# Performance work log

Measured on AMD Instinct MI355X. Metric: run time of the kernel, lower is better.

The kernel has to match this reference:

```python
import jax, jax.numpy as jnp
import numpy as np

N, E, D, H = 50000, 800000, 128, 8
C = D // H  # per-head out_channels = 16
NEG_SLOPE = 0.2
EPS = 1e-5


def _layer_norm(x, w):
    mu = x.mean(-1, keepdims=True)
    var = ((x - mu) ** 2).mean(-1, keepdims=True)
    return (x - mu) / jnp.sqrt(var + EPS) * w


def setup_inputs() -> dict:
    key = jax.random.key(0)
    ks = jax.random.split(key, 9)
    s = 0.05  # weight init scale
    return {
        "x": jax.random.normal(ks[0], (N, D), dtype=jnp.float32),
        "edge_index": jax.random.randint(ks[1], (2, E), 0, N, dtype=jnp.int32),
        "edge_attr": jax.random.normal(ks[2], (E, D), dtype=jnp.float32),
        "ln1_w": jnp.ones((D,), jnp.float32),
        "lin_l_w": jax.random.normal(ks[3], (D, D), dtype=jnp.float32) * s,
        "lin_l_b": jnp.zeros((D,), jnp.float32),
        "lin_r_w": jax.random.normal(ks[4], (D, D), dtype=jnp.float32) * s,
        "lin_r_b": jnp.zeros((D,), jnp.float32),
        "lin_edge_w": jax.random.normal(ks[5], (D, D), dtype=jnp.float32) * s,
        "att": jax.random.normal(ks[6], (H, C), dtype=jnp.float32) * s,
        "attn_bias": jnp.zeros((D,), jnp.float32),
        "ln2_w": jnp.ones((D,), jnp.float32),
        "fc_w": jax.random.normal(ks[7], (4 * D, D), dtype=jnp.float32) * s,
        "proj_w": jax.random.normal(ks[8], (D, 4 * D), dtype=jnp.float32) * s,
    }


def reference(x, edge_index, edge_attr, ln1_w, lin_l_w, lin_l_b, lin_r_w,
              lin_r_b, lin_edge_w, att, attn_bias, ln2_w, fc_w, proj_w):
    n, d = x.shape
    h_heads, c = att.shape
    # --- GATv2Conv on ln_1(x) ---
    h = _layer_norm(x, ln1_w)
    xl = (h @ lin_l_w.T + lin_l_b).reshape(n, h_heads, c)  # source transform
    xr = (h @ lin_r_w.T + lin_r_b).reshape(n, h_heads, c)  # target transform
    e = (edge_attr @ lin_edge_w.T).reshape(-1, h_heads, c)  # [E,H,C]
    src, dst = edge_index[0], edge_index[1]
    z = jax.nn.leaky_relu(xl[src] + xr[dst] + e, NEG_SLOPE)  # [E,H,C]
    logits = jnp.einsum('ehc,hc->eh', z, att)  # [E,H]
    # segment softmax over destination nodes
    m = jax.lax.stop_gradient(jax.ops.segment_max(logits, dst, num_segments=n))
    num = jnp.exp(logits - m[dst])
    den = jax.ops.segment_sum(num, dst, num_segments=n)
    alpha = num / den[dst]  # [E,H]
    msg = xl[src] * alpha[..., None]  # [E,H,C]
    attn_out = jax.ops.segment_sum(msg, dst, num_segments=n).reshape(n, d) + attn_bias
    x = x + attn_out
    # --- MLP on ln_2(x) ---
    h2 = _layer_norm(x, ln2_w)
    x = x + jax.nn.relu(h2 @ fc_w.T) @ proj_w.T
    return x
```

## Files before the change

### kernel.cpp

```cpp
#include <hip/hip_runtime.h>

#define D 128
#define HEADS 8
#define CH 16
#define NEG 0.2f
#define LNEPS 1e-5f

typedef __attribute__((ext_vector_type(8))) short bf16x8;
typedef __attribute__((ext_vector_type(4))) float f32x4;

#define MFMA(a, b, c) __builtin_amdgcn_mfma_f32_16x16x32_bf16(a, b, c, 0, 0, 0)

__device__ __forceinline__ short f2bf(float f) {
    unsigned u = __builtin_bit_cast(unsigned, f);
    unsigned r = (u + 0x7fffu + ((u >> 16) & 1u)) >> 16;
    return (short)r;
}
__device__ __forceinline__ float bflo(unsigned u) {
    return __builtin_bit_cast(float, u << 16);
}
__device__ __forceinline__ float bfhi(unsigned u) {
    return __builtin_bit_cast(float, u & 0xffff0000u);
}
__device__ __forceinline__ bf16x8 pack8(f32x4 lo, f32x4 hi) {
    bf16x8 r;
    r[0] = f2bf(lo[0]); r[1] = f2bf(lo[1]); r[2] = f2bf(lo[2]); r[3] = f2bf(lo[3]);
    r[4] = f2bf(hi[0]); r[5] = f2bf(hi[1]); r[6] = f2bf(hi[2]); r[7] = f2bf(hi[3]);
    return r;
}

__global__ void convert_weights(const float* __restrict__ wl, const float* __restrict__ wr,
                                const float* __restrict__ we, const float* __restrict__ fc,
                                const float* __restrict__ pj, short* __restrict__ out) {
    int idx = blockIdx.x * 256 + threadIdx.x;
    float v;
    if (idx < 16384) v = wl[idx];
    else if (idx < 32768) v = wr[idx - 16384];
    else if (idx < 49152) v = we[idx - 32768];
    else if (idx < 114688) v = fc[idx - 49152];
    else if (idx < 180224) v = pj[idx - 114688];
    else return;
    out[idx] = f2bf(v);
}

__global__ void ln_kernel(const float* __restrict__ x, const float* __restrict__ w,
                          short* __restrict__ h, int n) {
    int row = blockIdx.x * 4 + (threadIdx.x >> 6);
    if (row >= n) return;
    int l = threadIdx.x & 63;
    long base = (long)row * D;
    float a = x[base + l], b = x[base + l + 64];
    float s = a + b, ss = a * a + b * b;
    #pragma unroll
    for (int m = 1; m < 64; m <<= 1) { s += __shfl_xor(s, m); ss += __shfl_xor(ss, m); }
    float mu = s * (1.0f / 128.0f);
    float var = ss * (1.0f / 128.0f) - mu * mu;
    float rstd = rsqrtf(var + LNEPS);
    h[base + l]      = f2bf((a - mu) * rstd * w[l]);
    h[base + l + 64] = f2bf((b - mu) * rstd * w[l + 64]);
}

__global__ __launch_bounds__(256) void node_lin_kernel(
        const short* __restrict__ h, const short* __restrict__ wl, const short* __restrict__ wr,
        const float* __restrict__ bl, const float* __restrict__ br,
        short* __restrict__ xl, short* __restrict__ xr, int n) {
    int wave = threadIdx.x >> 6, l = threadIdx.x & 63;
    int rbase = blockIdx.x * 64 + wave * 16;
    int g = l >> 4, c = l & 15;
    f32x4 acc[16];
    #pragma unroll
    for (int t = 0; t < 16; t++) acc[t] = (f32x4){0.f, 0.f, 0.f, 0.f};
    int arow = rbase + c;
    #pragma unroll
    for (int kk = 0; kk < 4; kk++) {
        int k0 = kk * 32 + g * 8;
        bf16x8 af = {};
        if (arow < n) af = *(const bf16x8*)(h + (long)arow * D + k0);
        #pragma unroll
        for (int t = 0; t < 16; t++) {
            const short* w = (t < 8) ? wl : wr;
            int col = (t & 7) * 16 + c;
            bf16x8 bf = *(const bf16x8*)(w + col * D + k0);
            acc[t] = MFMA(af, bf, acc[t]);
        }
    }
    #pragma unroll
    for (int t = 0; t < 16; t++) {
        int col = (t & 7) * 16 + c;
        short* out = (t < 8) ? xl : xr;
        float bias = (t < 8) ? bl[col] : br[col];
        #pragma unroll
        for (int r = 0; r < 4; r++) {
            int row = rbase + g * 4 + r;
            if (row < n) out[(long)row * D + col] = f2bf(acc[t][r] + bias);
        }
    }
}

__global__ void hist_kernel(const int* __restrict__ dst, int* __restrict__ counts, int nE) {
    int e = blockIdx.x * 256 + threadIdx.x;
    if (e < nE) atomicAdd(&counts[dst[e]], 1);
}

__global__ void scan1_kernel(const int* __restrict__ counts, int* __restrict__ offsets,
                             int* __restrict__ blocksum, int n) {
    __shared__ int sd[1024];
    int tid = threadIdx.x;
    int gid = blockIdx.x * 1024 + tid;
    int v = (gid < n) ? counts[gid] : 0;
    sd[tid] = v;
    __syncthreads();
    int acc = v;
    #pragma unroll
    for (int off = 1; off < 1024; off <<= 1) {
        int t = (tid >= off) ? sd[tid - off] : 0;
        __syncthreads();
        acc += t;
        sd[tid] = acc;
        __syncthreads();
    }
    if (gid < n) offsets[gid] = acc - v;
    if (tid == 1023) blocksum[blockIdx.x] = acc;
}

__global__ void scan2_kernel(int* __restrict__ blocksum, int nb) {
    __shared__ int sd[256];
    int tid = threadIdx.x;
    int v = (tid < nb) ? blocksum[tid] : 0;
    sd[tid] = v;
    __syncthreads();
    int acc = v;
    #pragma unroll
    for (int off = 1; off < 256; off <<= 1) {
        int t = (tid >= off) ? sd[tid - off] : 0;
        __syncthreads();
        acc += t;
        sd[tid] = acc;
        __syncthreads();
    }
    if (tid < nb) blocksum[tid] = acc - v;
}

__global__ void scan3_kernel(int* __restrict__ offsets, const int* __restrict__ blocksum,
                             int* __restrict__ cursor, int n) {
    int gid = blockIdx.x * 256 + threadIdx.x;
    if (gid < n) {
        int o = offsets[gid] + blocksum[gid >> 10];
        offsets[gid] = o;
        cursor[gid] = o;
    }
}

__global__ void place_kernel(const int* __restrict__ src, const int* __restrict__ dst,
                             int* __restrict__ cursor, int* __restrict__ posOf,
                             int* __restrict__ src_perm, int nE) {
    int e = blockIdx.x * 256 + threadIdx.x;
    if (e < nE) {
        int pos = atomicAdd(&cursor[dst[e]], 1);
        posOf[e] = pos;
        src_perm[pos] = src[e];
    }
}

__global__ __launch_bounds__(256) void edge_kernel(
        const float* __restrict__ ea, const short* __restrict__ we,
        const int* __restrict__ src, const int* __restrict__ dst,
        const int* __restrict__ posOf,
        const short* __restrict__ xl, const short* __restrict__ xr,
        const float* __restrict__ att, float* __restrict__ num_perm,
        int nE, int ntiles, int nwaves) {
    __shared__ short wlds[16384];
    int tid = threadIdx.x;

    {
        int row = tid >> 1, half = tid & 1;
        const short* srow = we + row * D + half * 64;
        #pragma unroll
        for (int j = 0; j < 8; j++) {
            bf16x8 v = *(const bf16x8*)(srow + j * 8);
            int off = (half * 128 + j * 16) ^ ((row & 15) << 4);
            *(bf16x8*)((char*)wlds + row * 256 + off) = v;
        }
    }
    __syncthreads();

    int wave = tid >> 6, l = tid & 63;
    int el = l & 15, g = l >> 4;
    long ti = (long)blockIdx.x * 4 + wave;
    if (ti >= ntiles) return;

    int s, d, pos;
    f32x4 ear[8];
    {
        long e0 = ti * 16 + el;
        long ec = (e0 < nE) ? e0 : (nE - 1);
        s = src[ec]; d = dst[ec]; pos = posOf[ec];
        const float* p = ea + ec * D + g * 8;
        ear[0] = *(const f32x4*)(p);       ear[1] = *(const f32x4*)(p + 4);
        ear[2] = *(const f32x4*)(p + 32);  ear[3] = *(const f32x4*)(p + 36);
        ear[4] = *(const f32x4*)(p + 64);  ear[5] = *(const f32x4*)(p + 68);
        ear[6] = *(const f32x4*)(p + 96);  ear[7] = *(const f32x4*)(p + 100);
    }

    for (; ti < ntiles; ti += nwaves) {
        bool valid = (ti * 16 + el) < nE;
        int sc = s, dc = d, pc = pos;

        uint2 gl[8], gr[8];
        #pragma unroll
        for (int t = 0; t < 8; t++) {
            gl[t] = *(const uint2*)(xl + (long)sc * D + t * CH + g * 4);
            gr[t] = *(const uint2*)(xr + (long)dc * D + t * CH + g * 4);
        }

        long tin = ti + nwaves;
        long tcl = (tin < ntiles) ? tin : ti;
        long ecn;
        {
            long en = tcl * 16 + el;
            ecn = (en < nE) ? en : (nE - 1);
            s = src[ecn]; d = dst[ecn]; pos = posOf[ecn];
        }

        bf16x8 b0 = pack8(ear[0], ear[1]);
        bf16x8 b1 = pack8(ear[2], ear[3]);
        bf16x8 b2 = pack8(ear[4], ear[5]);
        bf16x8 b3 = pack8(ear[6], ear[7]);

        {
            const float* p = ea + ecn * D + g * 8;
            ear[0] = *(const f32x4*)(p);       ear[1] = *(const f32x4*)(p + 4);
            ear[2] = *(const f32x4*)(p + 32);  ear[3] = *(const f32x4*)(p + 36);
            ear[4] = *(const f32x4*)(p + 64);  ear[5] = *(const f32x4*)(p + 68);
            ear[6] = *(const f32x4*)(p + 96);  ear[7] = *(const f32x4*)(p + 100);
        }

        f32x4 acc[8];
        #pragma unroll
        for (int t = 0; t < 8; t++) acc[t] = (f32x4){0.f, 0.f, 0.f, 0.f};
        #pragma unroll
        for (int kk = 0; kk < 4; kk++) {
            bf16x8 bb = (kk == 0) ? b0 : (kk == 1) ? b1 : (kk == 2) ? b2 : b3;
            #pragma unroll
            for (int t = 0; t < 8; t++) {
                int row = t * CH + el;
                int off = row * 256 + ((kk * 64 + g * 16) ^ ((row & 15) << 4));
                bf16x8 af = *(const bf16x8*)((char*)wlds + off);
                acc[t] = MFMA(af, bb, acc[t]);
            }
        }

        float logit[8];
        #pragma unroll
        for (int t = 0; t < 8; t++) {
            f32x4 av = *(const f32x4*)(att + t * CH + g * 4);
            float v0 = acc[t][0] + bflo(gl[t].x) + bflo(gr[t].x);
            float v1 = acc[t][1] + bfhi(gl[t].x) + bfhi(gr[t].x);
            float v2 = acc[t][2] + bflo(gl[t].y) + bflo(gr[t].y);
            float v3 = acc[t][3] + bfhi(gl[t].y) + bfhi(gr[t].y);
            v0 = v0 > 0.f ? v0 : NEG * v0;
            v1 = v1 > 0.f ? v1 : NEG * v1;
            v2 = v2 > 0.f ? v2 : NEG * v2;
            v3 = v3 > 0.f ? v3 : NEG * v3;
            float lg = v0 * av[0];
            lg = fmaf(v1, av[1], lg);
            lg = fmaf(v2, av[2], lg);
            lg = fmaf(v3, av[3], lg);
            lg += __shfl_xor(lg, 16);
            lg += __shfl_xor(lg, 32);
            logit[t] = lg;
        }
        if (g == 0 && valid) {
            float4 o0 = make_float4(__expf(logit[0]), __expf(logit[1]),
                                    __expf(logit[2]), __expf(logit[3]));
            float4 o1 = make_float4(__expf(logit[4]), __expf(logit[5]),
                                    __expf(logit[6]), __expf(logit[7]));
            *(float4*)(num_perm + (long)pc * HEADS) = o0;
            *(float4*)(num_perm + (long)pc * HEADS + 4) = o1;
        }
    }
}

__global__ __launch_bounds__(256) void aggregate_kernel(
        const int* __restrict__ src_perm, const int* __restrict__ offsets,
        const int* __restrict__ counts, const float* __restrict__ num_perm,
        const short* __restrict__ xl, const float* __restrict__ x,
        const float* __restrict__ ab, const float* __restrict__ w2,
        float* __restrict__ x_mid, short* __restrict__ h2, int n) {
    int node = blockIdx.x * 4 + (threadIdx.x >> 6);
    if (node >= n) return;
    int l = threadIdx.x & 63;
    int h = l >> 3;
    int start = offsets[node], cnt = counts[node];
    float a0 = 0.f, a1 = 0.f, den = 0.f;
    int i = 0;
    for (; i + 4 <= cnt; i += 4) {
        int s0 = src_perm[start + i],     s1 = src_perm[start + i + 1];
        int s2 = src_perm[start + i + 2], s3 = src_perm[start + i + 3];
        float n0 = num_perm[(long)(start + i) * HEADS + h];
        float n1 = num_perm[(long)(start + i + 1) * HEADS + h];
        float n2 = num_perm[(long)(start + i + 2) * HEADS + h];
        float n3 = num_perm[(long)(start + i + 3) * HEADS + h];
        unsigned u0 = *(const unsigned*)(xl + (long)s0 * D + 2 * l);
        unsigned u1 = *(const unsigned*)(xl + (long)s1 * D + 2 * l);
        unsigned u2 = *(const unsigned*)(xl + (long)s2 * D + 2 * l);
        unsigned u3 = *(const unsigned*)(xl + (long)s3 * D + 2 * l);
        a0 = fmaf(bflo(u0), n0, a0); a1 = fmaf(bfhi(u0), n0, a1);
        a0 = fmaf(bflo(u1), n1, a0); a1 = fmaf(bfhi(u1), n1, a1);
        a0 = fmaf(bflo(u2), n2, a0); a1 = fmaf(bfhi(u2), n2, a1);
        a0 = fmaf(bflo(u3), n3, a0); a1 = fmaf(bfhi(u3), n3, a1);
        den += n0 + n1 + n2 + n3;
    }
    for (; i < cnt; i++) {
        float nm = num_perm[(long)(start + i) * HEADS + h];
        int s = src_perm[start + i];
        unsigned u = *(const unsigned*)(xl + (long)s * D + 2 * l);
        a0 = fmaf(bflo(u), nm, a0);
        a1 = fmaf(bfhi(u), nm, a1);
        den += nm;
    }
    float rden = cnt > 0 ? 1.f / den : 0.f;
    a0 *= rden; a1 *= rden;
    long base = (long)node * D;
    float2 xv = *(const float2*)(x + base + 2 * l);
    float2 abv = *(const float2*)(ab + 2 * l);
    float xm0 = xv.x + a0 + abv.x;
    float xm1 = xv.y + a1 + abv.y;
    *(float2*)(x_mid + base + 2 * l) = make_float2(xm0, xm1);
    float s_ = xm0 + xm1, ss = xm0 * xm0 + xm1 * xm1;
    #pragma unroll
    for (int m = 1; m < 64; m <<= 1) { s_ += __shfl_xor(s_, m); ss += __shfl_xor(ss, m); }
    float mu = s_ * (1.0f / 128.0f);
    float var = ss * (1.0f / 128.0f) - mu * mu;
    float rstd = rsqrtf(var + LNEPS);
    float2 wv = *(const float2*)(w2 + 2 * l);
    h2[base + 2 * l]     = f2bf((xm0 - mu) * rstd * wv.x);
    h2[base + 2 * l + 1] = f2bf((xm1 - mu) * rstd * wv.y);
}

__global__ __launch_bounds__(256) void fc_kernel(const short* __restrict__ h2,
                                                 const short* __restrict__ wfc,
                                                 short* __restrict__ t512, int n) {
    int wave = threadIdx.x >> 6, l = threadIdx.x & 63;
    int rbase = blockIdx.x * 64 + wave * 16;
    int cbase = blockIdx.y * 256;
    int g = l >> 4, c = l & 15;
    f32x4 acc[16];
    #pragma unroll
    for (int t = 0; t < 16; t++) acc[t] = (f32x4){0.f, 0.f, 0.f, 0.f};
    int arow = rbase + c;
    #pragma unroll
    for (int kk = 0; kk < 4; kk++) {
        int k0 = kk * 32 + g * 8;
        bf16x8 af = {};
        if (arow < n) af = *(const bf16x8*)(h2 + (long)arow * D + k0);
        #pragma unroll
        for (int t = 0; t < 16; t++) {
            int col = cbase + t * 16 + c;
            bf16x8 bf = *(const bf16x8*)(wfc + (long)col * D + k0);
            acc[t] = MFMA(af, bf, acc[t]);
        }
    }
    #pragma unroll
    for (int t = 0; t < 16; t++) {
        int col = cbase + t * 16 + c;
        #pragma unroll
        for (int r = 0; r < 4; r++) {
            int row = rbase + g * 4 + r;
            if (row < n) {
                float v = acc[t][r];
                t512[(long)row * 512 + col] = f2bf(v > 0.f ? v : 0.f);
            }
        }
    }
}

__global__ __launch_bounds__(256) void proj_kernel(const short* __restrict__ t512,
                                                   const short* __restrict__ wpj,
                                                   const float* __restrict__ x_mid,
                                                   float* __restrict__ out, int n) {
    int wave = threadIdx.x >> 6, l = threadIdx.x & 63;
    int rbase = blockIdx.x * 64 + wave * 16;
    int g = l >> 4, c = l & 15;
    f32x4 acc[8];
    #pragma unroll
    for (int t = 0; t < 8; t++) acc[t] = (f32x4){0.f, 0.f, 0.f, 0.f};
    int arow = rbase + c;
    #pragma unroll
    for (int kk = 0; kk < 16; kk++) {
        int k0 = kk * 32 + g * 8;
        bf16x8 af = {};
        if (arow < n) af = *(const bf16x8*)(t512 + (long)arow * 512 + k0);
        #pragma unroll
        for (int t = 0; t < 8; t++) {
            bf16x8 bf = *(const bf16x8*)(wpj + (long)(t * 16 + c) * 512 + k0);
            acc[t] = MFMA(af, bf, acc[t]);
        }
    }
    #pragma unroll
    for (int t = 0; t < 8; t++) {
        int col = t * 16 + c;
        #pragma unroll
        for (int r = 0; r < 4; r++) {
            int row = rbase + g * 4 + r;
            if (row < n) out[(long)row * D + col] = x_mid[(long)row * D + col] + acc[t][r];
        }
    }
}

extern "C" void kernel_launch(void* const* d_in, const int* in_sizes, int n_in,
                              void* d_out, int out_size, void* d_ws, size_t ws_size,
                              hipStream_t stream) {
    const float* x    = (const float*)d_in[0];
    const int*   eidx = (const int*)d_in[1];
    const float* ea   = (const float*)d_in[2];
    const float* ln1w = (const float*)d_in[3];
    const float* wl   = (const float*)d_in[4];
    const float* bl   = (const float*)d_in[5];
    const float* wr   = (const float*)d_in[6];
    const float* br   = (const float*)d_in[7];
    const float* we   = (const float*)d_in[8];
    const float* att  = (const float*)d_in[9];
    const float* ab   = (const float*)d_in[10];
    const float* ln2w = (const float*)d_in[11];
    const float* wfc  = (const float*)d_in[12];
    const float* wpj  = (const float*)d_in[13];
    int N = in_sizes[0] / D;
    int E = in_sizes[1] / 2;
    const int* srcp = eidx;
    const int* dstp = eidx + E;

    char* ws = (char*)d_ws;
    size_t NB2 = (size_t)N * D * 2;
    size_t NB4 = (size_t)N * D * 4;
    size_t E84 = (size_t)E * HEADS * 4;
    size_t o = 0;
    short* xl_bf   = (short*)(ws + o); o += NB2;
    short* xr_bf   = (short*)(ws + o); o += NB2;
    float* numperm = (float*)(ws + o); o += E84;
    float* xmid    = (float*)(ws + o); o += NB4;
    short* hbuf    = (short*)(ws + o); o += NB2;
    short* wbf     = (short*)(ws + o); o += 180224 * 2;
    int* counts    = (int*)(ws + o);   o += (size_t)N * 4;
    int* offsets   = (int*)(ws + o);   o += (size_t)N * 4;
    int* cursor    = (int*)(ws + o);   o += (size_t)N * 4;
    int* posOf     = (int*)(ws + o);   o += (size_t)E * 4;
    int* src_perm  = (int*)(ws + o);   o += (size_t)E * 4;
    int* blocksum  = (int*)(ws + o);   o += 256 * 4;
    short* t512    = (short*)ws;

    int nb = (N + 1023) / 1024;
    int ntiles = (E + 15) / 16;
    int egrid = 1280;
    int nwaves = egrid * 4;

    hipMemsetAsync(counts, 0, (size_t)N * 4, stream);

    convert_weights<<<704, 256, 0, stream>>>(wl, wr, we, wfc, wpj, wbf);
    ln_kernel<<<(N + 3) / 4, 256, 0, stream>>>(x, ln1w, hbuf, N);
    node_lin_kernel<<<(N + 63) / 64, 256, 0, stream>>>(hbuf, wbf, wbf + 16384,
                                                       bl, br, xl_bf, xr_bf, N);
    hist_kernel<<<(E + 255) / 256, 256, 0, stream>>>(dstp, counts, E);
    scan1_kernel<<<nb, 1024, 0, stream>>>(counts, offsets, blocksum, N);
    scan2_kernel<<<1, 256, 0, stream>>>(blocksum, nb);
    scan3_kernel<<<(N + 255) / 256, 256, 0, stream>>>(offsets, blocksum, cursor, N);
    place_kernel<<<(E + 255) / 256, 256, 0, stream>>>(srcp, dstp, cursor, posOf,
                                                      src_perm, E);
    edge_kernel<<<egrid, 256, 0, stream>>>(ea, wbf + 32768, srcp, dstp,
                                           posOf, xl_bf, xr_bf, att,
                                           numperm, E, ntiles, nwaves);
    aggregate_kernel<<<(N + 3) / 4, 256, 0, stream>>>(src_perm, offsets, counts,
                                                      numperm, xl_bf, x, ab, ln2w,
                                                      xmid, hbuf, N);
    fc_kernel<<<dim3((N + 63) / 64, 2), 256, 0, stream>>>(hbuf, wbf + 49152, t512, N);
    proj_kernel<<<(N + 63) / 64, 256, 0, stream>>>(t512, wbf + 114688, xmid,
                                                   (float*)d_out, N);
}
```

Baseline: 532.9 us.

## Fuse fc and proj through LDS; iterate edges in destination-sorted order

The MLP's fc and proj GEMMs are merged into one kernel. The ReLU'd 512-wide intermediate stays in a 64KB swizzled LDS tile instead of going to global memory, which removes the 51MB bf16 round trip and one launch. The edge kernel now walks edges in destination-sorted order, using new dst_perm and eid_perm arrays written by the place kernel. This makes xr gathers and num_perm writes sequential, but edge_attr reads become random-row gathers. The 64KB LDS per block limits occupancy of the fused MLP kernel.

```diff
diff --git a/kernel.cpp b/kernel.cpp
--- a/kernel.cpp
+++ b/kernel.cpp
@@ -152,20 +152,23 @@
 }
 
 __global__ void place_kernel(const int* __restrict__ src, const int* __restrict__ dst,
-                             int* __restrict__ cursor, int* __restrict__ posOf,
-                             int* __restrict__ src_perm, int nE) {
+                             int* __restrict__ cursor, int* __restrict__ src_perm,
+                             int* __restrict__ dst_perm, int* __restrict__ eid_perm,
+                             int nE) {
     int e = blockIdx.x * 256 + threadIdx.x;
     if (e < nE) {
-        int pos = atomicAdd(&cursor[dst[e]], 1);
-        posOf[e] = pos;
+        int d = dst[e];
+        int pos = atomicAdd(&cursor[d], 1);
         src_perm[pos] = src[e];
+        dst_perm[pos] = d;
+        eid_perm[pos] = e;
     }
 }
 
 __global__ __launch_bounds__(256) void edge_kernel(
         const float* __restrict__ ea, const short* __restrict__ we,
-        const int* __restrict__ src, const int* __restrict__ dst,
-        const int* __restrict__ posOf,
+        const int* __restrict__ src_perm, const int* __restrict__ dst_perm,
+        const int* __restrict__ eid_perm,
         const short* __restrict__ xl, const short* __restrict__ xr,
         const float* __restrict__ att, float* __restrict__ num_perm,
         int nE, int ntiles, int nwaves) {
@@ -189,13 +192,14 @@
     long ti = (long)blockIdx.x * 4 + wave;
     if (ti >= ntiles) return;
 
-    int s, d, pos;
+    int sp, dp;
     f32x4 ear[8];
     {
-        long e0 = ti * 16 + el;
-        long ec = (e0 < nE) ? e0 : (nE - 1);
-        s = src[ec]; d = dst[ec]; pos = posOf[ec];
-        const float* p = ea + ec * D + g * 8;
+        long p0 = ti * 16 + el;
+        long pc = (p0 < nE) ? p0 : (nE - 1);
+        sp = src_perm[pc]; dp = dst_perm[pc];
+        long ep = eid_perm[pc];
+        const float* p = ea + ep * D + g * 8;
         ear[0] = *(const f32x4*)(p);       ear[1] = *(const f32x4*)(p + 4);
         ear[2] = *(const f32x4*)(p + 32);  ear[3] = *(const f32x4*)(p + 36);
         ear[4] = *(const f32x4*)(p + 64);  ear[5] = *(const f32x4*)(p + 68);
@@ -203,8 +207,9 @@
     }
 
     for (; ti < ntiles; ti += nwaves) {
-        bool valid = (ti * 16 + el) < nE;
-        int sc = s, dc = d, pc = pos;
+        long pcur = ti * 16 + el;
+        bool valid = pcur < nE;
+        int sc = sp, dc = dp;
 
         uint2 gl[8], gr[8];
         #pragma unroll
@@ -215,11 +220,12 @@
 
         long tin = ti + nwaves;
         long tcl = (tin < ntiles) ? tin : ti;
-        long ecn;
+        long epn;
         {
-            long en = tcl * 16 + el;
-            ecn = (en < nE) ? en : (nE - 1);
-            s = src[ecn]; d = dst[ecn]; pos = posOf[ecn];
+            long pn = tcl * 16 + el;
+            long pc = (pn < nE) ? pn : (nE - 1);
+            sp = src_perm[pc]; dp = dst_perm[pc];
+            epn = eid_perm[pc];
         }
 
         bf16x8 b0 = pack8(ear[0], ear[1]);
@@ -228,7 +234,7 @@
         bf16x8 b3 = pack8(ear[6], ear[7]);
 
         {
-            const float* p = ea + ecn * D + g * 8;
+            const float* p = ea + epn * D + g * 8;
             ear[0] = *(const f32x4*)(p);       ear[1] = *(const f32x4*)(p + 4);
             ear[2] = *(const f32x4*)(p + 32);  ear[3] = *(const f32x4*)(p + 36);
             ear[4] = *(const f32x4*)(p + 64);  ear[5] = *(const f32x4*)(p + 68);
@@ -275,8 +281,8 @@
                                     __expf(logit[2]), __expf(logit[3]));
             float4 o1 = make_float4(__expf(logit[4]), __expf(logit[5]),
                                     __expf(logit[6]), __expf(logit[7]));
-            *(float4*)(num_perm + (long)pc * HEADS) = o0;
-            *(float4*)(num_perm + (long)pc * HEADS + 4) = o1;
+            *(float4*)(num_perm + pcur * HEADS) = o0;
+            *(float4*)(num_perm + pcur * HEADS + 4) = o1;
         }
     }
 }
@@ -338,63 +344,60 @@
     h2[base + 2 * l + 1] = f2bf((xm1 - mu) * rstd * wv.y);
 }
 
-__global__ __launch_bounds__(256) void fc_kernel(const short* __restrict__ h2,
-                                                 const short* __restrict__ wfc,
-                                                 short* __restrict__ t512, int n) {
-    int wave = threadIdx.x >> 6, l = threadIdx.x & 63;
-    int rbase = blockIdx.x * 64 + wave * 16;
-    int cbase = blockIdx.y * 256;
-    int g = l >> 4, c = l & 15;
-    f32x4 acc[16];
-    #pragma unroll
-    for (int t = 0; t < 16; t++) acc[t] = (f32x4){0.f, 0.f, 0.f, 0.f};
-    int arow = rbase + c;
-    #pragma unroll
-    for (int kk = 0; kk < 4; kk++) {
-        int k0 = kk * 32 + g * 8;
-        bf16x8 af = {};
-        if (arow < n) af = *(const bf16x8*)(h2 + (long)arow * D + k0);
-        #pragma unroll
-        for (int t = 0; t < 16; t++) {
-            int col = cbase + t * 16 + c;
-            bf16x8 bf = *(const bf16x8*)(wfc + (long)col * D + k0);
-            acc[t] = MFMA(af, bf, acc[t]);
-        }
-    }
-    #pragma unroll
-    for (int t = 0; t < 16; t++) {
-        int col = cbase + t * 16 + c;
-        #pragma unroll
-        for (int r = 0; r < 4; r++) {
-            int row = rbase + g * 4 + r;
-            if (row < n) {
-                float v = acc[t][r];
-                t512[(long)row * 512 + col] = f2bf(v > 0.f ? v : 0.f);
-            }
-        }
-    }
-}
-
-__global__ __launch_bounds__(256) void proj_kernel(const short* __restrict__ t512,
-                                                   const short* __restrict__ wpj,
-                                                   const float* __restrict__ x_mid,
-                                                   float* __restrict__ out, int n) {
+__global__ __launch_bounds__(256) void fcproj_kernel(
+        const short* __restrict__ h2, const short* __restrict__ wfc,
+        const short* __restrict__ wpj, const float* __restrict__ x_mid,
+        float* __restrict__ out, int n) {
+    __shared__ char tl[65536];
     int wave = threadIdx.x >> 6, l = threadIdx.x & 63;
     int rbase = blockIdx.x * 64 + wave * 16;
     int g = l >> 4, c = l & 15;
-    f32x4 acc[8];
-    #pragma unroll
-    for (int t = 0; t < 8; t++) acc[t] = (f32x4){0.f, 0.f, 0.f, 0.f};
     int arow = rbase + c;
+
+    #pragma unroll
+    for (int half = 0; half < 2; half++) {
+        f32x4 acc[16];
+        #pragma unroll
+        for (int t = 0; t < 16; t++) acc[t] = (f32x4){0.f, 0.f, 0.f, 0.f};
+        #pragma unroll
+        for (int kk = 0; kk < 4; kk++) {
+            int k0 = kk * 32 + g * 8;
+            bf16x8 af = {};
+            if (arow < n) af = *(const bf16x8*)(h2 + (long)arow * D + k0);
+            #pragma unroll
+            for (int t = 0; t < 16; t++) {
+                int col = half * 256 + t * 16 + c;
+                bf16x8 bf = *(const bf16x8*)(wfc + (long)col * D + k0);
+                acc[t] = MFMA(af, bf, acc[t]);
+            }
+        }
+        #pragma unroll
+        for (int t = 0; t < 16; t++) {
+            int col = half * 256 + t * 16 + c;
+            #pragma unroll
+            for (int r = 0; r < 4; r++) {
+                int lr = wave * 16 + g * 4 + r;
+                float v = acc[t][r];
+                int addr = lr * 1024 + ((2 * col) ^ ((lr & 7) << 4));
+                *(short*)(tl + addr) = f2bf(v > 0.f ? v : 0.f);
+            }
+        }
+    }
+    __syncthreads();
+
+    f32x4 pacc[8];
+    #pragma unroll
+    for (int t = 0; t < 8; t++) pacc[t] = (f32x4){0.f, 0.f, 0.f, 0.f};
+    int lr = wave * 16 + c;
     #pragma unroll
     for (int kk = 0; kk < 16; kk++) {
         int k0 = kk * 32 + g * 8;
-        bf16x8 af = {};
-        if (arow < n) af = *(const bf16x8*)(t512 + (long)arow * 512 + k0);
+        int addr = lr * 1024 + ((2 * k0) ^ ((lr & 7) << 4));
+        bf16x8 af = *(const bf16x8*)(tl + addr);
         #pragma unroll
         for (int t = 0; t < 8; t++) {
             bf16x8 bf = *(const bf16x8*)(wpj + (long)(t * 16 + c) * 512 + k0);
-            acc[t] = MFMA(af, bf, acc[t]);
+            pacc[t] = MFMA(af, bf, pacc[t]);
         }
     }
     #pragma unroll
@@ -403,7 +406,7 @@
         #pragma unroll
         for (int r = 0; r < 4; r++) {
             int row = rbase + g * 4 + r;
-            if (row < n) out[(long)row * D + col] = x_mid[(long)row * D + col] + acc[t][r];
+            if (row < n) out[(long)row * D + col] = x_mid[(long)row * D + col] + pacc[t][r];
         }
     }
 }
@@ -444,10 +447,10 @@
     int* counts    = (int*)(ws + o);   o += (size_t)N * 4;
     int* offsets   = (int*)(ws + o);   o += (size_t)N * 4;
     int* cursor    = (int*)(ws + o);   o += (size_t)N * 4;
-    int* posOf     = (int*)(ws + o);   o += (size_t)E * 4;
     int* src_perm  = (int*)(ws + o);   o += (size_t)E * 4;
+    int* dst_perm  = (int*)(ws + o);   o += (size_t)E * 4;
+    int* eid_perm  = (int*)(ws + o);   o += (size_t)E * 4;
     int* blocksum  = (int*)(ws + o);   o += 256 * 4;
-    short* t512    = (short*)ws;
 
     int nb = (N + 1023) / 1024;
     int ntiles = (E + 15) / 16;
@@ -464,15 +467,15 @@
     scan1_kernel<<<nb, 1024, 0, stream>>>(counts, offsets, blocksum, N);
     scan2_kernel<<<1, 256, 0, stream>>>(blocksum, nb);
     scan3_kernel<<<(N + 255) / 256, 256, 0, stream>>>(offsets, blocksum, cursor, N);
-    place_kernel<<<(E + 255) / 256, 256, 0, stream>>>(srcp, dstp, cursor, posOf,
-                                                      src_perm, E);
-    edge_kernel<<<egrid, 256, 0, stream>>>(ea, wbf + 32768, srcp, dstp,
-                                           posOf, xl_bf, xr_bf, att,
+    place_kernel<<<(E + 255) / 256, 256, 0, stream>>>(srcp, dstp, cursor, src_perm,
+                                                      dst_perm, eid_perm, E);
+    edge_kernel<<<egrid, 256, 0, stream>>>(ea, wbf + 32768, src_perm, dst_perm,
+                                           eid_perm, xl_bf, xr_bf, att,
                                            numperm, E, ntiles, nwaves);
     aggregate_kernel<<<(N + 3) / 4, 256, 0, stream>>>(src_perm, offsets, counts,
                                                       numperm, xl_bf, x, ab, ln2w,
                                                       xmid, hbuf, N);
-    fc_kernel<<<dim3((N + 63) / 64, 2), 256, 0, stream>>>(hbuf, wbf + 49152, t512, N);
-    proj_kernel<<<(N + 63) / 64, 256, 0, stream>>>(t512, wbf + 114688, xmid,
-                                                   (float*)d_out, N);
-}
+    fcproj_kernel<<<(N + 63) / 64, 256, 0, stream>>>(hbuf, wbf + 49152,
+                                                     wbf + 114688, xmid,
+                                                     (float*)d_out, N);
+}
```

Result: faster. 518.7 us (-2.7%).
